# Kernel tuning notes

Measured on AMD Instinct MI355X. Metric: run time of the kernel, lower is better.

The kernel has to match this reference:

```python
import jax, jax.numpy as jnp
import numpy as np


def setup_inputs() -> dict:
    key = jax.random.key(0)
    k_x, k_q, k_k, k_v = jax.random.split(key, 4)
    B, S, E, D = 4, 2048, 1024, 1024
    scale = 1.0 / np.sqrt(E)
    return {
        "x": jax.random.normal(k_x, (B, S, E), dtype=jnp.float32),
        # nn.Linear weight matrices, shape [out_dim, in_dim]; y = x @ W.T
        "w_q": jax.random.normal(k_q, (D, E), dtype=jnp.float32) * scale,
        "w_k": jax.random.normal(k_k, (D, E), dtype=jnp.float32) * scale,
        "w_v": jax.random.normal(k_v, (D, E), dtype=jnp.float32) * scale,
    }


def reference(x, w_q, w_k, w_v):
    # x: [B, S, E]; w_*: [D, E] (torch nn.Linear convention)
    B, S, E = x.shape
    q = jnp.einsum("bse,de->bsd", x, w_q)  # [B, S, D]
    k = jnp.einsum("bse,de->bsd", x, w_k)
    v = jnp.einsum("bse,de->bsd", x, w_v)
    D = q.shape[-1]
    # raw scores, then causal mask (strictly upper triangle -> -inf), then
    # scale by 1/sqrt(D) inside softmax exactly as the original does.
    scores = jnp.einsum("bsd,btd->bst", q, k)  # [B, S, S]
    causal = jnp.tril(jnp.ones((S, S), dtype=bool))  # True = keep
    scores = jnp.where(causal[None], scores, -jnp.inf)
    attn = jax.nn.softmax(scores / jnp.sqrt(jnp.asarray(D, x.dtype)), axis=-1)
    # dropout p=0.0 -> identity
    return jnp.einsum("bst,btd->bsd", attn, v)  # [B, S, D]
```

## Files before the change

### kernel.cpp

```cpp
#include <hip/hip_runtime.h>
#include <hip/hip_bf16.h>


typedef unsigned short u16;
typedef __attribute__((ext_vector_type(4))) u16   u16x4;
typedef __attribute__((ext_vector_type(8))) u16   u16x8;
typedef __attribute__((ext_vector_type(8))) short short8;
typedef __attribute__((ext_vector_type(4))) float f32x4;
typedef __attribute__((ext_vector_type(4))) int   i32x4;

__device__ inline u16 f2b(float v) {
    __hip_bfloat16 b = __float2bfloat16(v);
    return *reinterpret_cast<u16*>(&b);
}
__device__ inline float b2f(u16 v) {
    unsigned int u = ((unsigned int)v) << 16;
    return *reinterpret_cast<float*>(&u);
}

template <typename T> __device__ inline void store_elem(T* p, float v);
template <> __device__ inline void store_elem<float>(float* p, float v) { *p = v; }
template <> __device__ inline void store_elem<u16>(u16* p, float v)     { *p = f2b(v); }

__device__ inline void gload_lds16(const u16* g, u16* l) {
    __builtin_amdgcn_global_load_lds(
        (const __attribute__((address_space(1))) void*)g,
        (__attribute__((address_space(3))) void*)l, 16, 0, 0);
}

__global__ __launch_bounds__(256) void cast_all_kernel(
    const float* __restrict__ x,  const float* __restrict__ wq,
    const float* __restrict__ wk, const float* __restrict__ wv,
    u16* __restrict__ dst) {
    int q = blockIdx.x * 256 + threadIdx.x;
    const float* src;
    int sidx;
    if (q < 2097152) { src = x; sidx = q * 4; }
    else {
        int qq = q - 2097152;
        int w  = qq >> 18;
        sidx   = (qq & 262143) * 4;
        src    = (w == 0) ? wq : (w == 1) ? wk : wv;
    }
    float4 v = *(const float4*)(src + sidx);
    u16x4 o;
    o.x = f2b(v.x); o.y = f2b(v.y); o.z = f2b(v.z); o.w = f2b(v.w);
    *(u16x4*)(dst + q * 4) = o;
}

__device__ __forceinline__ void gemm256_core(
    u16* __restrict__ lds,
    const u16* __restrict__ Ab, int lda,
    const u16* __restrict__ Bb, int ldb,
    u16* __restrict__ Cb, int ldc,
    int m0, int n0)
{
    const int tid  = threadIdx.x;
    const int lane = tid & 63;
    const int wave = tid >> 6;
    const int quad = lane >> 4;
    const int r16  = lane & 15;
    const int wm   = wave >> 2;
    const int wn   = wave & 3;

    int gA[2][2], gB[2][2], lA[2][2], lB[2][2];
    {
        const int cswz = ((lane & 3) * 8) ^ (((lane >> 5) & 1) << 4);
        const int rsub = lane >> 2;
#pragma unroll
        for (int u = 0; u < 2; ++u)
#pragma unroll
            for (int j = 0; j < 2; ++j) {
                int s   = j * 8 + wave;
                int sh  = s >> 1, cg = s & 1;
                int rgA = (sh & 3) + (sh >> 2) * 8 + u * 4;
                int rgB = sh + u * 8;
                int cl  = cg * 32 + cswz;
                gA[u][j] = (m0 + rgA * 16 + rsub) * lda + cl;
                gB[u][j] = (n0 + rgB * 16 + rsub) * ldb + cl;
                lA[u][j] = (rgA * 2 + cg) * 512 + lane * 8;
                lB[u][j] = (rgB * 2 + cg) * 512 + lane * 8;
            }
    }

#define STAGE_A(BUF, U, KK) do { \
        gload_lds16(Ab + gA[U][0] + (KK), lds + (BUF)*32768 + lA[U][0]); \
        gload_lds16(Ab + gA[U][1] + (KK), lds + (BUF)*32768 + lA[U][1]); } while (0)
#define STAGE_B(BUF, U, KK) do { \
        gload_lds16(Bb + gB[U][0] + (KK), lds + (BUF)*32768 + 16384 + lB[U][0]); \
        gload_lds16(Bb + gB[U][1] + (KK), lds + (BUF)*32768 + 16384 + lB[U][1]); } while (0)

    const int cswr = (quad * 8) ^ ((r16 >> 3) << 4);
    const int rdA0 = wm * 16 * 512 + r16 * 32 + cswr;
    const int rdB0 = wn * 8  * 512 + r16 * 32 + cswr;

    f32x4 acc[8][4] = {};

    STAGE_B(0, 0, 0);  STAGE_B(0, 1, 0);  STAGE_A(0, 0, 0);  STAGE_A(0, 1, 0);
    STAGE_B(1, 0, 64); STAGE_B(1, 1, 64); STAGE_A(1, 0, 64); STAGE_A(1, 1, 64);
    asm volatile("s_waitcnt vmcnt(8)" ::: "memory");
    __builtin_amdgcn_s_barrier();

    for (int t = 0; t < 16; ++t) {
        const int  buf = t & 1;
        const int  kk2 = t * 64 + 128;
        const bool pf  = (t < 14);
        const u16* Al  = lds + buf * 32768;
        const u16* Bl  = lds + buf * 32768 + 16384;
        short8 bfr[4][2], a01[2][2], a23[2][2], a45[2][2], a67[2][2];

#pragma unroll
        for (int nf = 0; nf < 4; ++nf)
#pragma unroll
            for (int ks = 0; ks < 2; ++ks)
                bfr[nf][ks] = *(const short8*)&Bl[rdB0 + (nf * 2 + ks) * 512];
#pragma unroll
        for (int mf = 0; mf < 2; ++mf)
#pragma unroll
            for (int ks = 0; ks < 2; ++ks)
                a01[mf][ks] = *(const short8*)&Al[rdA0 + (mf * 2 + ks) * 512];
        __builtin_amdgcn_s_barrier();
        __builtin_amdgcn_s_setprio(1);
#pragma unroll
        for (int mf = 0; mf < 2; ++mf)
#pragma unroll
            for (int nf = 0; nf < 4; ++nf)
#pragma unroll
                for (int ks = 0; ks < 2; ++ks)
                    acc[mf][nf] = __builtin_amdgcn_mfma_f32_16x16x32_bf16(
                        a01[mf][ks], bfr[nf][ks], acc[mf][nf], 0, 0, 0);
        __builtin_amdgcn_s_setprio(0);
        __builtin_amdgcn_s_barrier();

#pragma unroll
        for (int mf = 0; mf < 2; ++mf)
#pragma unroll
            for (int ks = 0; ks < 2; ++ks)
                a23[mf][ks] = *(const short8*)&Al[rdA0 + ((mf + 2) * 2 + ks) * 512];
        if (pf) STAGE_B(buf, 0, kk2);
        __builtin_amdgcn_s_barrier();
        __builtin_amdgcn_s_setprio(1);
#pragma unroll
        for (int mf = 0; mf < 2; ++mf)
#pragma unroll
            for (int nf = 0; nf < 4; ++nf)
#pragma unroll
                for (int ks = 0; ks < 2; ++ks)
                    acc[mf + 2][nf] = __builtin_amdgcn_mfma_f32_16x16x32_bf16(
                        a23[mf][ks], bfr[nf][ks], acc[mf + 2][nf], 0, 0, 0);
        __builtin_amdgcn_s_setprio(0);
        __builtin_amdgcn_s_barrier();

#pragma unroll
        for (int mf = 0; mf < 2; ++mf)
#pragma unroll
            for (int ks = 0; ks < 2; ++ks) {
                a45[mf][ks] = *(const short8*)&Al[rdA0 + ((mf + 4) * 2 + ks) * 512];
                a67[mf][ks] = *(const short8*)&Al[rdA0 + ((mf + 6) * 2 + ks) * 512];
            }
        if (pf) STAGE_B(buf, 1, kk2);
        __builtin_amdgcn_s_barrier();
        __builtin_amdgcn_s_setprio(1);
#pragma unroll
        for (int mf = 0; mf < 2; ++mf)
#pragma unroll
            for (int nf = 0; nf < 4; ++nf)
#pragma unroll
                for (int ks = 0; ks < 2; ++ks)
                    acc[mf + 4][nf] = __builtin_amdgcn_mfma_f32_16x16x32_bf16(
                        a45[mf][ks], bfr[nf][ks], acc[mf + 4][nf], 0, 0, 0);
        __builtin_amdgcn_s_setprio(0);
        asm volatile("s_waitcnt lgkmcnt(0)" ::: "memory");
        __builtin_amdgcn_s_barrier();

        if (pf) { STAGE_A(buf, 0, kk2); STAGE_A(buf, 1, kk2); }
        __builtin_amdgcn_s_barrier();
        __builtin_amdgcn_s_setprio(1);
#pragma unroll
        for (int mf = 0; mf < 2; ++mf)
#pragma unroll
            for (int nf = 0; nf < 4; ++nf)
#pragma unroll
                for (int ks = 0; ks < 2; ++ks)
                    acc[mf + 6][nf] = __builtin_amdgcn_mfma_f32_16x16x32_bf16(
                        a67[mf][ks], bfr[nf][ks], acc[mf + 6][nf], 0, 0, 0);
        __builtin_amdgcn_s_setprio(0);
        if (pf) asm volatile("s_waitcnt vmcnt(8)" ::: "memory");
        else    asm volatile("s_waitcnt vmcnt(0)" ::: "memory");
        __builtin_amdgcn_s_barrier();
    }
#undef STAGE_A
#undef STAGE_B

#pragma unroll
    for (int mf = 0; mf < 8; ++mf) {
        int m = m0 + wm * 128 + mf * 16 + quad * 4;
#pragma unroll
        for (int nf = 0; nf < 4; ++nf) {
            int n = n0 + wn * 64 + nf * 16 + r16;
#pragma unroll
            for (int r = 0; r < 4; ++r)
                Cb[(m + r) * ldc + n] = f2b(acc[mf][nf][r]);
        }
    }
}

__global__ __launch_bounds__(512) void gemm_qk256(
    const u16* __restrict__ xb, const u16* __restrict__ wb,
    u16* __restrict__ qk)
{
    __shared__ __align__(16) u16 lds[2 * 2 * 16384];
    int flat = blockIdx.x;
    int swz  = (flat & 7) * 32 + (flat >> 3);
    int m0   = (swz >> 3) * 256;
    int n0   = (swz & 7) * 256;
    gemm256_core(lds, xb, 1024, wb, 1024, qk, 2048, m0, n0);
}

__global__ __launch_bounds__(512) void gemm_sc256(
    const u16* __restrict__ qk, u16* __restrict__ sc)
{
    __shared__ __align__(16) u16 lds[2 * 2 * 16384];
    int flat = blockIdx.x;
    int swz  = (flat & 7) * 18 + (flat >> 3);
    int z    = swz / 36;
    int t    = swz - z * 36;
    float ff = sqrtf(8.0f * t + 1.0f);
    int m = (int)((ff - 1.0f) * 0.5f);
    while ((m + 1) * (m + 2) / 2 <= t) m++;
    while (m * (m + 1) / 2 > t) m--;
    int n = t - m * (m + 1) / 2;
    const u16* Ab = qk + (long long)z * 2048 * 2048;
    gemm256_core(lds, Ab, 2048, Ab + 1024, 2048,
                 sc + (long long)z * 2048 * 2048, 2048, m * 256, n * 256);
}

#define MT 128
#define NT 128
#define BKH 32
#define HSZ (MT * BKH)

template <int TRANS, typename OutT>
__device__ __forceinline__ void gemm_core(
    u16* __restrict__ As, u16* __restrict__ Bs,
    const u16* __restrict__ Ab, int lda,
    const u16* __restrict__ Bb, int ldb,
    OutT* __restrict__ Cb, int ldc,
    int m0, int n0, int kbeg, int kend)
{
    const int tid  = threadIdx.x;
    const int lane = tid & 63;
    const int wave = tid >> 6;
    const int quad = lane >> 4;
    const int r16  = lane & 15;
    const int mw   = (wave >> 1) * 64;
    const int nw   = (wave & 1) * 64;

    const int c0 = tid, c1 = tid + 256;
    const int r0 = c0 >> 2, k0 = (c0 & 3) * 8;
    const int r1 = c1 >> 2, k1 = (c1 & 3) * 8;
    const int oa0 = (m0 + r0) * lda + k0;
    const int oa1 = (m0 + r1) * lda + k1;
    const int ob0 = (n0 + r0) * ldb + k0;
    const int ob1 = (n0 + r1) * ldb + k1;

    f32x4 acc[4][4] = {};

    for (int kk = kbeg; kk < kend; kk += 2 * BKH) {
        __syncthreads();
        gload_lds16(Ab + (kk + oa0),        &As[c0 * 8]);
        gload_lds16(Ab + (kk + oa1),        &As[c1 * 8]);
        gload_lds16(Ab + (kk + BKH + oa0),  &As[HSZ + c0 * 8]);
        gload_lds16(Ab + (kk + BKH + oa1),  &As[HSZ + c1 * 8]);
        gload_lds16(Bb + (kk + ob0),        &Bs[c0 * 8]);
        gload_lds16(Bb + (kk + ob1),        &Bs[c1 * 8]);
        gload_lds16(Bb + (kk + BKH + ob0),  &Bs[HSZ + c0 * 8]);
        gload_lds16(Bb + (kk + BKH + ob1),  &Bs[HSZ + c1 * 8]);
        __syncthreads();

#pragma unroll
        for (int h = 0; h < 2; h++) {
            short8 af[4], bf[4];
#pragma unroll
            for (int i = 0; i < 4; i++)
                af[i] = *(const short8*)&As[h * HSZ + (mw + i * 16 + r16) * BKH + quad * 8];
#pragma unroll
            for (int j = 0; j < 4; j++)
                bf[j] = *(const short8*)&Bs[h * HSZ + (nw + j * 16 + r16) * BKH + quad * 8];
#pragma unroll
            for (int i = 0; i < 4; i++)
#pragma unroll
                for (int j = 0; j < 4; j++)
                    acc[i][j] = __builtin_amdgcn_mfma_f32_16x16x32_bf16(af[i], bf[j], acc[i][j], 0, 0, 0);
        }
    }

    if (TRANS == 0) {
#pragma unroll
        for (int i = 0; i < 4; i++)
#pragma unroll
            for (int j = 0; j < 4; j++)
#pragma unroll
                for (int r = 0; r < 4; r++) {
                    int m = m0 + mw + i * 16 + quad * 4 + r;
                    int n = n0 + nw + j * 16 + r16;
                    store_elem(&Cb[(long long)m * ldc + n], acc[i][j][r]);
                }
    } else {
#pragma unroll
        for (int i = 0; i < 4; i++)
#pragma unroll
            for (int j = 0; j < 4; j++) {
                int mbase = m0 + mw + i * 16 + quad * 4;
                int d     = n0 + nw + j * 16 + r16;
                int b     = mbase >> 11;
                int s     = mbase & 2047;
                u16x4 o;
#pragma unroll
                for (int r = 0; r < 4; r++) o[r] = f2b(acc[i][j][r]);
                *(u16x4*)((u16*)Cb + (((b << 10) + d) * 2048 + s)) = o;
            }
    }
}

__device__ __forceinline__ void softmax_row(const u16* __restrict__ sc,
                                            u16* __restrict__ P, int row,
                                            float* __restrict__ red) {
    const int S = 2048;
    int i   = row & (S - 1);
    int n   = i + 1;
    int kendr = (i & ~127) + 128;
    const u16* srow = sc + (long long)row * S;
    u16*       prow = P  + (long long)row * S;

    int j0 = threadIdx.x * 8;
    u16x8 raw = {};
    if (j0 <= i) raw = *(const u16x8*)(srow + j0);
    float v[8];
#pragma unroll
    for (int e = 0; e < 8; e++) v[e] = (j0 + e < n) ? b2f(raw[e]) : -1e30f;

    float lmax = v[0];
#pragma unroll
    for (int e = 1; e < 8; e++) lmax = fmaxf(lmax, v[e]);
    for (int o = 32; o > 0; o >>= 1) lmax = fmaxf(lmax, __shfl_xor(lmax, o, 64));
    int wid = threadIdx.x >> 6;
    if ((threadIdx.x & 63) == 0) red[wid] = lmax;
    __syncthreads();
    float Mx = fmaxf(fmaxf(red[0], red[1]), fmaxf(red[2], red[3]));

    const float C = 0.045112384f;
    float ev[8];
    float lsum = 0.f;
#pragma unroll
    for (int e = 0; e < 8; e++) {
        ev[e] = (j0 + e < n) ? exp2f((v[e] - Mx) * C) : 0.f;
        lsum += ev[e];
    }
    for (int o = 32; o > 0; o >>= 1) lsum += __shfl_xor(lsum, o, 64);
    if ((threadIdx.x & 63) == 0) red[4 + wid] = lsum;
    __syncthreads();
    float inv = 1.0f / (red[4] + red[5] + red[6] + red[7]);

    if (j0 < kendr) {
        u16x8 o8;
#pragma unroll
        for (int e = 0; e < 8; e++) o8[e] = f2b(ev[e] * inv);
        *(u16x8*)(prow + j0) = o8;
    }
}

__global__ __launch_bounds__(256, 4) void v_softmax(
    const u16* __restrict__ xb, const u16* __restrict__ wb,
    u16* __restrict__ vt,
    const u16* __restrict__ sc, u16* __restrict__ P)
{
    __shared__ __align__(16) u16 As[2 * HSZ];
    __shared__ __align__(16) u16 Bs[2 * HSZ];
    int bid = blockIdx.x;
    if (bid < 512) {
        int vb = (bid & 7) * 64 + (bid >> 3);
        int m0 = (vb >> 3) * MT;
        int n0 = (vb & 7) * NT;
        gemm_core<1, u16>(As, Bs, xb, 1024, wb + 2048 * 1024, 1024, vt, 2048,
                          m0, n0, 0, 1024);
    } else {
        float* red = (float*)As;
        int sid = bid - 512;
        int z = sid >> 10, i = sid & 1023;
        softmax_row(sc, P, z * 2048 + (2047 - i), red);
        softmax_row(sc, P, z * 2048 + i, red);
    }
}

__global__ __launch_bounds__(256, 4) void gemm_pv(
    const u16* __restrict__ P, const u16* __restrict__ vt,
    float* __restrict__ out, float* __restrict__ part)
{
    __shared__ __align__(16) u16 As[2 * HSZ];
    __shared__ __align__(16) u16 Bs[2 * HSZ];
    const int bid = blockIdx.x;
    int m, chunk, n;
    if (bid < 80) {
        int q = bid >> 3; n = bid & 7;
        if (q < 9) { m = 7 + q; chunk = 0; } else { m = 15; chunk = 1; }
    } else {
        int r = bid - 80; int s = 7 - (r >> 4); int t = r & 15;
        n = t & 7;
        if (t < 8) { m = s - 1; chunk = 0; } else { m = s + 7; chunk = 1; }
    }
    const int m0 = m * MT, n0 = n * NT;
    const int kbeg = chunk ? 1024 : 0;
    const int kend = chunk ? (m0 + MT) : min(1024, m0 + MT);
    const int b = blockIdx.z;

    const u16* Ab = P  + (long long)b * 2048 * 2048;
    const u16* Bb = vt + (long long)b * 1024 * 2048;
    float* Cb = (chunk == 0)
        ? out  + (long long)b * 2097152
        : part + (long long)b * 1048576 - 1024LL * 1024;
    gemm_core<0, float>(As, Bs, Ab, 2048, Bb, 2048, Cb, 1024, m0, n0, kbeg, kend);
}

__global__ __launch_bounds__(256) void pv_combine(float* __restrict__ out,
                                                  const float* __restrict__ part) {
    long long idx = ((long long)blockIdx.x * 256 + threadIdx.x) * 8;
    long long bb = idx >> 20;
    long long j  = idx & 1048575;
    float* o = out + bb * 2097152 + 1048576 + j;
    const float* p = part + bb * 1048576 + j;
    float4 o0 = *(float4*)o, o1 = *(float4*)(o + 4);
    float4 p0 = *(const float4*)p, p1 = *(const float4*)(p + 4);
    o0.x += p0.x; o0.y += p0.y; o0.z += p0.z; o0.w += p0.w;
    o1.x += p1.x; o1.y += p1.y; o1.z += p1.z; o1.w += p1.w;
    *(float4*)o = o0; *(float4*)(o + 4) = o1;
}

extern "C" void kernel_launch(void* const* d_in, const int* in_sizes, int n_in,
                              void* d_out, int out_size, void* d_ws, size_t ws_size,
                              hipStream_t stream) {
    const float* x  = (const float*)d_in[0];
    const float* wq = (const float*)d_in[1];
    const float* wk = (const float*)d_in[2];
    const float* wv = (const float*)d_in[3];
    float* out = (float*)d_out;

    char* ws = (char*)d_ws;
    u16*   xb   = (u16*)(ws);
    u16*   wb   = (u16*)(ws + 16777216LL);
    u16*   qk   = (u16*)(ws + 23068672LL);
    u16*   sc   = (u16*)(ws + 56623104LL);
    u16*   P    = (u16*)(ws + 90177536LL);
    u16*   vt   = (u16*)(ws + 123731968LL);
    float* part = (float*)(ws + 140509184LL);

    cast_all_kernel<<<11264, 256, 0, stream>>>(x, wq, wk, wv, xb);

    gemm_qk256<<<256, 512, 0, stream>>>(xb, wb, qk);

    gemm_sc256<<<144, 512, 0, stream>>>(qk, sc);

    v_softmax<<<4608, 256, 0, stream>>>(xb, wb, vt, sc, P);

    gemm_pv<<<dim3(192, 1, 4), 256, 0, stream>>>(P, vt, out, part);
    pv_combine<<<2048, 256, 0, stream>>>(out, part);
}
```

Before: 235.5 us.

## Split PV GEMM into balanced K-chunks with atomic accumulation, drop combine kernel

The PV GEMM now uses a table-driven split-K schedule with finer chunks of 128-wide K blocks, 34 work units per batch, to balance the causal triangle across blocks. Partial results are accumulated directly into the output with float atomics, which removes the separate partial buffer and the pv_combine kernel. The output is zeroed by extra blocks appended to the scores GEMM launch. In exchange, every output element pays atomic-add traffic, and summation order becomes nondeterministic.

```diff
diff --git a/kernel.cpp b/kernel.cpp
--- a/kernel.cpp
+++ b/kernel.cpp
@@ -7,7 +7,6 @@
 typedef __attribute__((ext_vector_type(8))) u16   u16x8;
 typedef __attribute__((ext_vector_type(8))) short short8;
 typedef __attribute__((ext_vector_type(4))) float f32x4;
-typedef __attribute__((ext_vector_type(4))) int   i32x4;
 
 __device__ inline u16 f2b(float v) {
     __hip_bfloat16 b = __float2bfloat16(v);
@@ -17,10 +16,6 @@
     unsigned int u = ((unsigned int)v) << 16;
     return *reinterpret_cast<float*>(&u);
 }
-
-template <typename T> __device__ inline void store_elem(T* p, float v);
-template <> __device__ inline void store_elem<float>(float* p, float v) { *p = v; }
-template <> __device__ inline void store_elem<u16>(u16* p, float v)     { *p = f2b(v); }
 
 __device__ inline void gload_lds16(const u16* g, u16* l) {
     __builtin_amdgcn_global_load_lds(
@@ -218,10 +213,20 @@
 }
 
 __global__ __launch_bounds__(512) void gemm_sc256(
-    const u16* __restrict__ qk, u16* __restrict__ sc)
+    const u16* __restrict__ qk, u16* __restrict__ sc,
+    float* __restrict__ out)
 {
     __shared__ __align__(16) u16 lds[2 * 2 * 16384];
     int flat = blockIdx.x;
+    if (flat >= 144) {
+        int zb = flat - 144;
+        long long base = (long long)zb * 8192 + threadIdx.x * 4;
+        float4 z4 = {0.f, 0.f, 0.f, 0.f};
+#pragma unroll
+        for (int r = 0; r < 4; ++r)
+            *(float4*)(out + base + r * 2048) = z4;
+        return;
+    }
     int swz  = (flat & 7) * 18 + (flat >> 3);
     int z    = swz / 36;
     int t    = swz - z * 36;
@@ -240,7 +245,7 @@
 #define BKH 32
 #define HSZ (MT * BKH)
 
-template <int TRANS, typename OutT>
+template <int TRANS, int ATOMIC, typename OutT>
 __device__ __forceinline__ void gemm_core(
     u16* __restrict__ As, u16* __restrict__ Bs,
     const u16* __restrict__ Ab, int lda,
@@ -304,7 +309,11 @@
                 for (int r = 0; r < 4; r++) {
                     int m = m0 + mw + i * 16 + quad * 4 + r;
                     int n = n0 + nw + j * 16 + r16;
-                    store_elem(&Cb[(long long)m * ldc + n], acc[i][j][r]);
+                    if (ATOMIC)
+                        unsafeAtomicAdd((float*)&Cb[(long long)m * ldc + n],
+                                        acc[i][j][r]);
+                    else
+                        Cb[(long long)m * ldc + n] = (OutT)acc[i][j][r];
                 }
     } else {
 #pragma unroll
@@ -382,8 +391,8 @@
         int vb = (bid & 7) * 64 + (bid >> 3);
         int m0 = (vb >> 3) * MT;
         int n0 = (vb & 7) * NT;
-        gemm_core<1, u16>(As, Bs, xb, 1024, wb + 2048 * 1024, 1024, vt, 2048,
-                          m0, n0, 0, 1024);
+        gemm_core<1, 0, u16>(As, Bs, xb, 1024, wb + 2048 * 1024, 1024, vt, 2048,
+                             m0, n0, 0, 1024);
     } else {
         float* red = (float*)As;
         int sid = bid - 512;
@@ -393,47 +402,33 @@
     }
 }
 
+__device__ const unsigned char PV_M[34] =
+    {4,8,9,9,12,13,13,14,14,14, 3,6,7,7,8,10,10,11,11,11,12,12,13,15,15,15,15,
+     2,5,5,6,10, 1,0};
+__device__ const unsigned char PV_KB[34] =
+    {0,0,0,5,0,0,5,0,5,10, 0,0,0,4,5,0,4,0,4,8,5,9,10,0,4,8,12, 0,0,3,4,8, 0,0};
+__device__ const unsigned char PV_KE[34] =
+    {5,5,5,10,5,5,10,5,10,15, 4,4,4,8,9,4,8,4,8,12,9,13,14,4,8,12,16,
+     3,3,6,7,11, 2,1};
+
 __global__ __launch_bounds__(256, 4) void gemm_pv(
     const u16* __restrict__ P, const u16* __restrict__ vt,
-    float* __restrict__ out, float* __restrict__ part)
+    float* __restrict__ out)
 {
     __shared__ __align__(16) u16 As[2 * HSZ];
     __shared__ __align__(16) u16 Bs[2 * HSZ];
-    const int bid = blockIdx.x;
-    int m, chunk, n;
-    if (bid < 80) {
-        int q = bid >> 3; n = bid & 7;
-        if (q < 9) { m = 7 + q; chunk = 0; } else { m = 15; chunk = 1; }
-    } else {
-        int r = bid - 80; int s = 7 - (r >> 4); int t = r & 15;
-        n = t & 7;
-        if (t < 8) { m = s - 1; chunk = 0; } else { m = s + 7; chunk = 1; }
-    }
-    const int m0 = m * MT, n0 = n * NT;
-    const int kbeg = chunk ? 1024 : 0;
-    const int kend = chunk ? (m0 + MT) : min(1024, m0 + MT);
+    const int u = blockIdx.x >> 3;
+    const int n = blockIdx.x & 7;
+    const int m    = PV_M[u];
+    const int kbeg = PV_KB[u] * 128;
+    const int kend = PV_KE[u] * 128;
     const int b = blockIdx.z;
 
-    const u16* Ab = P  + (long long)b * 2048 * 2048;
-    const u16* Bb = vt + (long long)b * 1024 * 2048;
-    float* Cb = (chunk == 0)
-        ? out  + (long long)b * 2097152
-        : part + (long long)b * 1048576 - 1024LL * 1024;
-    gemm_core<0, float>(As, Bs, Ab, 2048, Bb, 2048, Cb, 1024, m0, n0, kbeg, kend);
-}
-
-__global__ __launch_bounds__(256) void pv_combine(float* __restrict__ out,
-                                                  const float* __restrict__ part) {
-    long long idx = ((long long)blockIdx.x * 256 + threadIdx.x) * 8;
-    long long bb = idx >> 20;
-    long long j  = idx & 1048575;
-    float* o = out + bb * 2097152 + 1048576 + j;
-    const float* p = part + bb * 1048576 + j;
-    float4 o0 = *(float4*)o, o1 = *(float4*)(o + 4);
-    float4 p0 = *(const float4*)p, p1 = *(const float4*)(p + 4);
-    o0.x += p0.x; o0.y += p0.y; o0.z += p0.z; o0.w += p0.w;
-    o1.x += p1.x; o1.y += p1.y; o1.z += p1.z; o1.w += p1.w;
-    *(float4*)o = o0; *(float4*)(o + 4) = o1;
+    gemm_core<0, 1, float>(As, Bs,
+        P  + (long long)b * 2048 * 2048, 2048,
+        vt + (long long)b * 1024 * 2048, 2048,
+        out + (long long)b * 2097152, 1024,
+        m * MT, n * NT, kbeg, kend);
 }
 
 extern "C" void kernel_launch(void* const* d_in, const int* in_sizes, int n_in,
@@ -452,16 +447,14 @@
     u16*   sc   = (u16*)(ws + 56623104LL);
     u16*   P    = (u16*)(ws + 90177536LL);
     u16*   vt   = (u16*)(ws + 123731968LL);
-    float* part = (float*)(ws + 140509184LL);
 
     cast_all_kernel<<<11264, 256, 0, stream>>>(x, wq, wk, wv, xb);
 
     gemm_qk256<<<256, 512, 0, stream>>>(xb, wb, qk);
 
-    gemm_sc256<<<144, 512, 0, stream>>>(qk, sc);
+    gemm_sc256<<<1168, 512, 0, stream>>>(qk, sc, out);
 
     v_softmax<<<4608, 256, 0, stream>>>(xb, wb, vt, sc, P);
 
-    gemm_pv<<<dim3(192, 1, 4), 256, 0, stream>>>(P, vt, out, part);
-    pv_combine<<<2048, 256, 0, stream>>>(out, part);
-}
+    gemm_pv<<<dim3(272, 1, 4), 256, 0, stream>>>(P, vt, out);
+}
```

New measurement: 258.2 us. 9.7% more time.

## Drop split-K in PV GEMM and order tiles longest-first

Applied to the files above, without the earlier changes.

Removes the split-K decomposition of the P·V GEMM and the separate pv_combine kernel. Each of the 512 blocks now computes a full causal K range for one output tile, and blocks are ordered so the longest row tiles are scheduled first. This eliminates the partial-sum buffer round trip and one kernel launch, but lengthens the critical path of the largest tiles, since no tile's K loop is split any more.

```diff
diff --git a/kernel.cpp b/kernel.cpp
--- a/kernel.cpp
+++ b/kernel.cpp
@@ -7,7 +7,6 @@
 typedef __attribute__((ext_vector_type(8))) u16   u16x8;
 typedef __attribute__((ext_vector_type(8))) short short8;
 typedef __attribute__((ext_vector_type(4))) float f32x4;
-typedef __attribute__((ext_vector_type(4))) int   i32x4;
 
 __device__ inline u16 f2b(float v) {
     __hip_bfloat16 b = __float2bfloat16(v);
@@ -395,45 +394,22 @@
 
 __global__ __launch_bounds__(256, 4) void gemm_pv(
     const u16* __restrict__ P, const u16* __restrict__ vt,
-    float* __restrict__ out, float* __restrict__ part)
+    float* __restrict__ out)
 {
     __shared__ __align__(16) u16 As[2 * HSZ];
     __shared__ __align__(16) u16 Bs[2 * HSZ];
     const int bid = blockIdx.x;
-    int m, chunk, n;
-    if (bid < 80) {
-        int q = bid >> 3; n = bid & 7;
-        if (q < 9) { m = 7 + q; chunk = 0; } else { m = 15; chunk = 1; }
-    } else {
-        int r = bid - 80; int s = 7 - (r >> 4); int t = r & 15;
-        n = t & 7;
-        if (t < 8) { m = s - 1; chunk = 0; } else { m = s + 7; chunk = 1; }
-    }
-    const int m0 = m * MT, n0 = n * NT;
-    const int kbeg = chunk ? 1024 : 0;
-    const int kend = chunk ? (m0 + MT) : min(1024, m0 + MT);
-    const int b = blockIdx.z;
-
-    const u16* Ab = P  + (long long)b * 2048 * 2048;
-    const u16* Bb = vt + (long long)b * 1024 * 2048;
-    float* Cb = (chunk == 0)
-        ? out  + (long long)b * 2097152
-        : part + (long long)b * 1048576 - 1024LL * 1024;
-    gemm_core<0, float>(As, Bs, Ab, 2048, Bb, 2048, Cb, 1024, m0, n0, kbeg, kend);
-}
-
-__global__ __launch_bounds__(256) void pv_combine(float* __restrict__ out,
-                                                  const float* __restrict__ part) {
-    long long idx = ((long long)blockIdx.x * 256 + threadIdx.x) * 8;
-    long long bb = idx >> 20;
-    long long j  = idx & 1048575;
-    float* o = out + bb * 2097152 + 1048576 + j;
-    const float* p = part + bb * 1048576 + j;
-    float4 o0 = *(float4*)o, o1 = *(float4*)(o + 4);
-    float4 p0 = *(const float4*)p, p1 = *(const float4*)(p + 4);
-    o0.x += p0.x; o0.y += p0.y; o0.z += p0.z; o0.w += p0.w;
-    o1.x += p1.x; o1.y += p1.y; o1.z += p1.z; o1.w += p1.w;
-    *(float4*)o = o0; *(float4*)(o + 4) = o1;
+    const int m  = (bid < 256) ? (15 - (bid >> 5)) : ((bid - 256) >> 5);
+    const int nz = bid & 31;
+    const int n  = nz & 7;
+    const int z  = nz >> 3;
+    const int m0 = m * MT;
+
+    gemm_core<0, float>(As, Bs,
+        P  + (long long)z * 2048 * 2048, 2048,
+        vt + (long long)z * 1024 * 2048, 2048,
+        out + (long long)z * 2097152, 1024,
+        m0, n * NT, 0, m0 + MT);
 }
 
 extern "C" void kernel_launch(void* const* d_in, const int* in_sizes, int n_in,
@@ -452,7 +428,6 @@
     u16*   sc   = (u16*)(ws + 56623104LL);
     u16*   P    = (u16*)(ws + 90177536LL);
     u16*   vt   = (u16*)(ws + 123731968LL);
-    float* part = (float*)(ws + 140509184LL);
 
     cast_all_kernel<<<11264, 256, 0, stream>>>(x, wq, wk, wv, xb);
 
@@ -462,6 +437,5 @@
 
     v_softmax<<<4608, 256, 0, stream>>>(xb, wb, vt, sc, P);
 
-    gemm_pv<<<dim3(192, 1, 4), 256, 0, stream>>>(P, vt, out, part);
-    pv_combine<<<2048, 256, 0, stream>>>(out, part);
-}
+    gemm_pv<<<512, 256, 0, stream>>>(P, vt, out);
+}
```

Result: faster. 230.4 us (-2.2%).
